# Kernel tuning notes

Measured on AMD Instinct MI355X. Metric: run time of the kernel, lower is better.

## Reference

```python
import jax, jax.numpy as jnp
import numpy as np

B, N, E = 4, 1024, 8192
NF_IN, NF_H, NF_OUT = 32, 128, 3


def _lin(key, fan_in, fan_out):
    k1, k2 = jax.random.split(key)
    bound = 1.0 / np.sqrt(fan_in)
    W = jax.random.uniform(k1, (fan_in, fan_out), jnp.float32, -bound, bound)
    b = jax.random.uniform(k2, (fan_out,), jnp.float32, -bound, bound)
    return W, b


def setup_inputs() -> dict:
    key = jax.random.key(0)
    ks = jax.random.split(key, 16)
    x = jax.random.normal(ks[0], (B, N, NF_IN), jnp.float32)
    # One-hot receiver/sender relation matrices [B, E, N]
    recv = jax.random.randint(ks[1], (B, E), 0, N)
    send = jax.random.randint(ks[2], (B, E), 0, N)
    Rr = jax.nn.one_hot(recv, N, dtype=jnp.float32)
    Rs = jax.nn.one_hot(send, N, dtype=jnp.float32)
    neW0, neb0 = _lin(ks[3], NF_IN, NF_H)
    neW1, neb1 = _lin(ks[4], NF_H, NF_H)
    neW2, neb2 = _lin(ks[5], NF_H, NF_H)
    eeW0, eeb0 = _lin(ks[6], NF_IN * 2, NF_H)
    eeW1, eeb1 = _lin(ks[7], NF_H, NF_H)
    eeW2, eeb2 = _lin(ks[8], NF_H, NF_H)
    npW, npb = _lin(ks[9], NF_H * 2, NF_H)
    epW, epb = _lin(ks[10], NF_H * 3, NF_H)
    ppW0, ppb0 = _lin(ks[11], NF_H * 2, NF_H)
    ppW1, ppb1 = _lin(ks[12], NF_H, NF_H)
    ppW2, ppb2 = _lin(ks[13], NF_H, NF_OUT)
    return dict(x=x, Rr=Rr, Rs=Rs, pstep=2,
                neW0=neW0, neb0=neb0, neW1=neW1, neb1=neb1, neW2=neW2, neb2=neb2,
                eeW0=eeW0, eeb0=eeb0, eeW1=eeW1, eeb1=eeb1, eeW2=eeW2, eeb2=eeb2,
                npW=npW, npb=npb, epW=epW, epb=epb,
                ppW0=ppW0, ppb0=ppb0, ppW1=ppW1, ppb1=ppb1, ppW2=ppW2, ppb2=ppb2)


def _encoder(x, W0, b0, W1, b1, W2, b2):
    # Linear->ReLU x3 (ReLU after last layer too)
    h = jax.nn.relu(x @ W0 + b0)
    h = jax.nn.relu(h @ W1 + b1)
    return jax.nn.relu(h @ W2 + b2)


def _predictor(x, W0, b0, W1, b1, W2, b2):
    h = jax.nn.relu(x @ W0 + b0)
    h = jax.nn.relu(h @ W1 + b1)
    return h @ W2 + b2


def reference(x, Rr, Rs, pstep,
              neW0, neb0, neW1, neb1, neW2, neb2,
              eeW0, eeb0, eeW1, eeb1, eeW2, eeb2,
              npW, npb, epW, epb,
              ppW0, ppb0, ppW1, ppb1, ppW2, ppb2):
    node_encode = _encoder(x, neW0, neb0, neW1, neb1, neW2, neb2)  # [B,N,H]
    node_effect = node_encode
    x_r = jnp.einsum('ben,bnf->bef', Rr, x)  # gather receiver features
    x_s = jnp.einsum('ben,bnf->bef', Rs, x)  # gather sender features
    edge_encode = _encoder(jnp.concatenate([x_r, x_s], -1),
                           eeW0, eeb0, eeW1, eeb1, eeW2, eeb2)  # [B,E,H]
    for _ in range(pstep):
        ne_r = jnp.einsum('ben,bnh->beh', Rr, node_effect)
        ne_s = jnp.einsum('ben,bnh->beh', Rs, node_effect)
        edge_in = jnp.concatenate([edge_encode, ne_r, ne_s], -1)  # [B,E,3H]
        edge_effect = jax.nn.relu(edge_in @ epW + epb)  # [B,E,H]
        agg = jnp.einsum('ben,beh->bnh', Rr, edge_effect)  # scatter-add to receivers
        node_in = jnp.concatenate([node_encode, agg], -1)  # [B,N,2H]
        node_effect = jax.nn.relu(node_in @ npW + npb + node_effect)  # residual
    node_reps = _predictor(jnp.concatenate([node_encode, node_effect], -1),
                           ppW0, ppb0, ppW1, ppb1, ppW2, ppb2)  # [B,N,out]
    return node_reps
```

## Files before the change

### kernel.cpp

```cpp
#include <hip/hip_runtime.h>
#include <hip/hip_bf16.h>


typedef unsigned short u16;
typedef __attribute__((ext_vector_type(8))) __bf16 bf16x8;
typedef __attribute__((ext_vector_type(4))) float f32x4;

#define N_    1024
#define BN    4096
#define BE    32768
#define LOG_E 13
#define H_    128
#define LSTR  132
#define ECAP  64
#define ASTR  136

__device__ __forceinline__ u16 f2bf(float f) {
    __bf16 h = (__bf16)f;
    return __builtin_bit_cast(u16, h);
}

__device__ __forceinline__ bf16x8 cvt8(float4 f0, float4 f1) {
    bf16x8 a;
    a[0] = (__bf16)f0.x; a[1] = (__bf16)f0.y; a[2] = (__bf16)f0.z; a[3] = (__bf16)f0.w;
    a[4] = (__bf16)f1.x; a[5] = (__bf16)f1.y; a[6] = (__bf16)f1.z; a[7] = (__bf16)f1.w;
    return a;
}

__device__ __forceinline__ bf16x8 a_from_f32(const float* p) {
    float4 f0 = *(const float4*)p;
    float4 f1 = *(const float4*)(p + 4);
    return cvt8(f0, f1);
}

__device__ __forceinline__ bf16x8 a_from_lds(const float* lds, int r, int quad, int c) {
    return a_from_f32(lds + r * LSTR + c * 32 + quad * 8);
}

__device__ __forceinline__ void mm2(const u16* __restrict__ Wf, int c, int ntb,
                                    bf16x8 a, f32x4* acc, int lane) {
    const u16* wp = Wf + ((size_t)c * 8) * 64 * 8;
    #pragma unroll
    for (int nt = 0; nt < 2; ++nt) {
        bf16x8 bw = *(const bf16x8*)(wp + (size_t)((ntb + nt) * 64 + lane) * 8);
        acc[nt] = __builtin_amdgcn_mfma_f32_16x16x32_bf16(a, bw, acc[nt], 0, 0, 0);
    }
}

__device__ __forceinline__ void zacc2(f32x4* acc) {
    acc[0] = (f32x4){0.f, 0.f, 0.f, 0.f};
    acc[1] = (f32x4){0.f, 0.f, 0.f, 0.f};
}

__device__ __forceinline__ void epi2_lds(float* lds, const f32x4* acc,
                                         const float* __restrict__ bias,
                                         int quad, int m, int ntb) {
    #pragma unroll
    for (int nt = 0; nt < 2; ++nt) {
        int col = (ntb + nt) * 16 + m;
        float bv = bias[col];
        #pragma unroll
        for (int i = 0; i < 4; ++i)
            lds[(quad * 4 + i) * LSTR + col] = fmaxf(acc[nt][i] + bv, 0.f);
    }
}

struct WDesc { const float* src; u16* dst; int K; };
struct WPack { WDesc d[10]; };

__global__ __launch_bounds__(256) void k_prep(WPack P,
                                              const float* __restrict__ Rr,
                                              const float* __restrict__ Rs,
                                              int* __restrict__ recv,
                                              int* __restrict__ send,
                                              int* __restrict__ deg,
                                              int* __restrict__ eidx) {
    int bx = blockIdx.x;
    if (bx >= 16384) {
        int t = bx - 16384;
        WDesc d = P.d[t / 192];
        int i = (t % 192) * 256 + threadIdx.x;
        if (i >= d.K * 128) return;
        int j    = i & 7;
        int lane = (i >> 3) & 63;
        int nt   = (i >> 9) & 7;
        int c    = i >> 12;
        int k = c * 32 + (lane >> 4) * 8 + j;
        int n = nt * 16 + (lane & 15);
        d.dst[i] = f2bf(d.src[k * 128 + n]);
        return;
    }
    int wave = threadIdx.x >> 6, lane = threadIdx.x & 63;
    int g = bx * 4 + wave;
    const float* src;
    int* dst;
    if (g < BE) { src = Rr + (size_t)g * N_;        dst = recv + g; }
    else        { src = Rs + (size_t)(g - BE) * N_; dst = send + (g - BE); }
    int idx = 0;
    bool done = false;
    #pragma unroll
    for (int it = 0; it < 4; ++it) {
        if (!done) {
            int base = it * 256 + lane * 4;
            float4 v = *(const float4*)(src + base);
            int found = -1;
            if      (v.x != 0.f) found = base;
            else if (v.y != 0.f) found = base + 1;
            else if (v.z != 0.f) found = base + 2;
            else if (v.w != 0.f) found = base + 3;
            unsigned long long msk = __ballot(found >= 0);
            if (msk) {
                int sl = __ffsll((long long)msk) - 1;
                idx = __shfl(found, sl, 64);
                done = true;
            }
        }
    }
    if (lane == 0) {
        *dst = idx;
        if (g < BE) {
            int node = (g >> LOG_E) * N_ + idx;
            int pos = atomicAdd(deg + node, 1);
            if (pos < ECAP) eidx[node * ECAP + pos] = g;
        }
    }
}

__global__ __launch_bounds__(256) void k_enc(
    const float* __restrict__ x,
    const int* __restrict__ recv, const int* __restrict__ send,
    const u16* __restrict__ nW0, const float* __restrict__ nb0,
    const u16* __restrict__ nW1, const float* __restrict__ nb1,
    const u16* __restrict__ nW2, const float* __restrict__ nb2,
    const u16* __restrict__ eW0, const float* __restrict__ eb0,
    const u16* __restrict__ eW1, const float* __restrict__ eb1,
    const u16* __restrict__ eW2, const float* __restrict__ eb2,
    float* __restrict__ nenc_f, u16* __restrict__ nenc_bf,
    u16* __restrict__ eenc)
{
    __shared__ float lds[2][16 * LSTR];
    int tid = threadIdx.x, lane = tid & 63, w = tid >> 6;
    int m = lane & 15, quad = lane >> 4;
    int ntb = w * 2;
    f32x4 acc[2];

    if (blockIdx.x < 256) {
        int row16 = blockIdx.x * 16;
        zacc2(acc);
        mm2(nW0, 0, ntb, a_from_f32(x + (size_t)(row16 + m) * 32 + quad * 8), acc, lane);
        epi2_lds(lds[0], acc, nb0, quad, m, ntb);
        __syncthreads();

        zacc2(acc);
        #pragma unroll
        for (int c = 0; c < 4; ++c)
            mm2(nW1, c, ntb, a_from_lds(lds[0], m, quad, c), acc, lane);
        epi2_lds(lds[1], acc, nb1, quad, m, ntb);
        __syncthreads();

        zacc2(acc);
        #pragma unroll
        for (int c = 0; c < 4; ++c)
            mm2(nW2, c, ntb, a_from_lds(lds[1], m, quad, c), acc, lane);
        epi2_lds(lds[0], acc, nb2, quad, m, ntb);
        __syncthreads();

        #pragma unroll
        for (int t = 0; t < 8; ++t) {
            int flat = t * 256 + tid, r = flat >> 7, col = flat & 127;
            nenc_f[(size_t)(row16 + r) * H_ + col] = lds[0][r * LSTR + col];
        }
        #pragma unroll
        for (int t = 0; t < 4; ++t) {
            int p = t * 256 + tid, r = p >> 6, c2 = (p & 63) * 2;
            u16 lo = f2bf(lds[0][r * LSTR + c2]);
            u16 hi = f2bf(lds[0][r * LSTR + c2 + 1]);
            *(unsigned*)(nenc_bf + (size_t)(row16 + r) * H_ + c2) =
                (unsigned)lo | ((unsigned)hi << 16);
        }
        return;
    }

    int row16 = (blockIdx.x - 256) * 16;
    int e = row16 + m, b = e >> LOG_E;
    long rr = (long)b * N_ + recv[e];
    long rs = (long)b * N_ + send[e];

    zacc2(acc);
    mm2(eW0, 0, ntb, a_from_f32(x + rr * 32 + quad * 8), acc, lane);
    mm2(eW0, 1, ntb, a_from_f32(x + rs * 32 + quad * 8), acc, lane);
    epi2_lds(lds[0], acc, eb0, quad, m, ntb);
    __syncthreads();

    zacc2(acc);
    #pragma unroll
    for (int c = 0; c < 4; ++c)
        mm2(eW1, c, ntb, a_from_lds(lds[0], m, quad, c), acc, lane);
    epi2_lds(lds[1], acc, eb1, quad, m, ntb);
    __syncthreads();

    zacc2(acc);
    #pragma unroll
    for (int c = 0; c < 4; ++c)
        mm2(eW2, c, ntb, a_from_lds(lds[1], m, quad, c), acc, lane);
    epi2_lds(lds[0], acc, eb2, quad, m, ntb);
    __syncthreads();

    #pragma unroll
    for (int t = 0; t < 4; ++t) {
        int p = t * 256 + tid, r = p >> 6, c2 = (p & 63) * 2;
        u16 lo = f2bf(lds[0][r * LSTR + c2]);
        u16 hi = f2bf(lds[0][r * LSTR + c2 + 1]);
        *(unsigned*)(eenc + (size_t)(row16 + r) * H_ + c2) =
            (unsigned)lo | ((unsigned)hi << 16);
    }
}

__global__ __launch_bounds__(256) void k_eprop(
    const u16* __restrict__ eenc, const u16* __restrict__ eff_bf,
    const int* __restrict__ recv, const int* __restrict__ send,
    const u16* __restrict__ Wf, const float* __restrict__ bias,
    float* __restrict__ edge_eff)
{
    int tid = threadIdx.x, lane = tid & 63, w = tid >> 6;
    int m = lane & 15, quad = lane >> 4;
    int row16 = blockIdx.x * 16, ntb = w * 2;
    int e = row16 + m;
    long rr = ((long)(e >> LOG_E) * N_ + recv[e]) * H_;
    long rs = ((long)(e >> LOG_E) * N_ + send[e]) * H_;
    f32x4 acc[2];
    zacc2(acc);

    #pragma unroll
    for (int c = 0; c < 4; ++c)
        mm2(Wf, c, ntb,
            *(const bf16x8*)(eenc + (size_t)e * H_ + c * 32 + quad * 8), acc, lane);
    #pragma unroll
    for (int c = 0; c < 4; ++c)
        mm2(Wf, 4 + c, ntb,
            *(const bf16x8*)(eff_bf + rr + c * 32 + quad * 8), acc, lane);
    #pragma unroll
    for (int c = 0; c < 4; ++c)
        mm2(Wf, 8 + c, ntb,
            *(const bf16x8*)(eff_bf + rs + c * 32 + quad * 8), acc, lane);

    #pragma unroll
    for (int nt = 0; nt < 2; ++nt) {
        int col = (ntb + nt) * 16 + m;
        float bv = bias[col];
        #pragma unroll
        for (int i = 0; i < 4; ++i)
            edge_eff[(size_t)(row16 + quad * 4 + i) * H_ + col] =
                fmaxf(acc[nt][i] + bv, 0.f);
    }
}

__device__ __forceinline__ void gather_agg(u16* aggl, int row16, int tid, int lane,
                                           const float* __restrict__ edge_eff,
                                           const int* __restrict__ deg,
                                           const int* __restrict__ eidx) {
    int nd = tid >> 4, l = tid & 15;
    int node = row16 + nd;
    int dg = deg[node]; dg = dg < ECAP ? dg : ECAP;
    int ev = eidx[node * ECAP + l];
    int base = lane & 48;
    float s[8] = {0.f, 0.f, 0.f, 0.f, 0.f, 0.f, 0.f, 0.f};
    int d16 = dg < 16 ? dg : 16;
    int t = 0;
    for (; t + 1 < d16; t += 2) {
        int e0 = __shfl(ev, base | t, 64);
        int e1 = __shfl(ev, base | (t + 1), 64);
        const float* p0 = edge_eff + (size_t)e0 * H_ + l * 8;
        const float* p1 = edge_eff + (size_t)e1 * H_ + l * 8;
        float4 a0 = *(const float4*)p0, b0 = *(const float4*)(p0 + 4);
        float4 a1 = *(const float4*)p1, b1 = *(const float4*)(p1 + 4);
        s[0] += a0.x + a1.x; s[1] += a0.y + a1.y;
        s[2] += a0.z + a1.z; s[3] += a0.w + a1.w;
        s[4] += b0.x + b1.x; s[5] += b0.y + b1.y;
        s[6] += b0.z + b1.z; s[7] += b0.w + b1.w;
    }
    if (t < d16) {
        int e0 = __shfl(ev, base | t, 64);
        const float* p0 = edge_eff + (size_t)e0 * H_ + l * 8;
        float4 a0 = *(const float4*)p0, b0 = *(const float4*)(p0 + 4);
        s[0] += a0.x; s[1] += a0.y; s[2] += a0.z; s[3] += a0.w;
        s[4] += b0.x; s[5] += b0.y; s[6] += b0.z; s[7] += b0.w;
        ++t;
    }
    for (; t < dg; ++t) {
        int e0 = eidx[node * ECAP + t];
        const float* p0 = edge_eff + (size_t)e0 * H_ + l * 8;
        float4 a0 = *(const float4*)p0, b0 = *(const float4*)(p0 + 4);
        s[0] += a0.x; s[1] += a0.y; s[2] += a0.z; s[3] += a0.w;
        s[4] += b0.x; s[5] += b0.y; s[6] += b0.z; s[7] += b0.w;
    }
    bf16x8 o;
    #pragma unroll
    for (int j = 0; j < 8; ++j) o[j] = (__bf16)s[j];
    *(bf16x8*)(aggl + nd * ASTR + l * 8) = o;
}

__global__ __launch_bounds__(256) void k_nprop(
    const u16* __restrict__ nenc_bf, const float* __restrict__ edge_eff,
    const int* __restrict__ deg, const int* __restrict__ eidx,
    const float* __restrict__ eff_f,
    const u16* __restrict__ Wf, const float* __restrict__ bias,
    float* __restrict__ nout_f, u16* __restrict__ nout_bf)
{
    __shared__ u16 aggl[16 * ASTR];
    int tid = threadIdx.x, lane = tid & 63, w = tid >> 6;
    int m = lane & 15, quad = lane >> 4;
    int row16 = blockIdx.x * 16;

    gather_agg(aggl, row16, tid, lane, edge_eff, deg, eidx);
    __syncthreads();

    int row = row16 + m, ntb = w * 2;
    f32x4 acc[2];
    zacc2(acc);
    #pragma unroll
    for (int c = 0; c < 4; ++c)
        mm2(Wf, c, ntb,
            *(const bf16x8*)(nenc_bf + (size_t)row * H_ + c * 32 + quad * 8), acc, lane);
    #pragma unroll
    for (int c = 0; c < 4; ++c)
        mm2(Wf, 4 + c, ntb,
            *(const bf16x8*)(aggl + m * ASTR + c * 32 + quad * 8), acc, lane);

    #pragma unroll
    for (int nt = 0; nt < 2; ++nt) {
        int col = (ntb + nt) * 16 + m;
        float bv = bias[col];
        #pragma unroll
        for (int i = 0; i < 4; ++i) {
            int r = row16 + quad * 4 + i;
            float v = fmaxf(acc[nt][i] + bv + eff_f[(size_t)r * H_ + col], 0.f);
            nout_f[(size_t)r * H_ + col] = v;
            nout_bf[(size_t)r * H_ + col] = f2bf(v);
        }
    }
}

__global__ __launch_bounds__(256) void k_npropred(
    const u16* __restrict__ nenc_bf, const float* __restrict__ edge_eff,
    const int* __restrict__ deg, const int* __restrict__ eidx,
    const float* __restrict__ eff_f,
    const u16* __restrict__ Wnp, const float* __restrict__ bnp,
    const u16* __restrict__ Wp0, const float* __restrict__ bp0,
    const u16* __restrict__ Wp1, const float* __restrict__ bp1,
    const float* __restrict__ W2, const float* __restrict__ b2,
    float* __restrict__ out)
{
    __shared__ u16 aggl[16 * ASTR];
    __shared__ u16 vl[16 * ASTR];
    __shared__ u16 h1[16 * ASTR];
    __shared__ float h2[16 * LSTR];
    int tid = threadIdx.x, lane = tid & 63, w = tid >> 6;
    int m = lane & 15, quad = lane >> 4;
    int row16 = blockIdx.x * 16;

    gather_agg(aggl, row16, tid, lane, edge_eff, deg, eidx);
    __syncthreads();

    int row = row16 + m, ntb = w * 2;
    f32x4 acc[2];

    zacc2(acc);
    #pragma unroll
    for (int c = 0; c < 4; ++c)
        mm2(Wnp, c, ntb,
            *(const bf16x8*)(nenc_bf + (size_t)row * H_ + c * 32 + quad * 8), acc, lane);
    #pragma unroll
    for (int c = 0; c < 4; ++c)
        mm2(Wnp, 4 + c, ntb,
            *(const bf16x8*)(aggl + m * ASTR + c * 32 + quad * 8), acc, lane);
    #pragma unroll
    for (int nt = 0; nt < 2; ++nt) {
        int col = (ntb + nt) * 16 + m;
        float bv = bnp[col];
        #pragma unroll
        for (int i = 0; i < 4; ++i) {
            int r = quad * 4 + i;
            float v = fmaxf(acc[nt][i] + bv + eff_f[(size_t)(row16 + r) * H_ + col], 0.f);
            vl[r * ASTR + col] = f2bf(v);
        }
    }
    __syncthreads();

    zacc2(acc);
    #pragma unroll
    for (int c = 0; c < 4; ++c)
        mm2(Wp0, c, ntb,
            *(const bf16x8*)(nenc_bf + (size_t)row * H_ + c * 32 + quad * 8), acc, lane);
    #pragma unroll
    for (int c = 0; c < 4; ++c)
        mm2(Wp0, 4 + c, ntb,
            *(const bf16x8*)(vl + m * ASTR + c * 32 + quad * 8), acc, lane);
    #pragma unroll
    for (int nt = 0; nt < 2; ++nt) {
        int col = (ntb + nt) * 16 + m;
        float bv = bp0[col];
        #pragma unroll
        for (int i = 0; i < 4; ++i)
            h1[(quad * 4 + i) * ASTR + col] = f2bf(fmaxf(acc[nt][i] + bv, 0.f));
    }
    __syncthreads();

    zacc2(acc);
    #pragma unroll
    for (int c = 0; c < 4; ++c)
        mm2(Wp1, c, ntb,
            *(const bf16x8*)(h1 + m * ASTR + c * 32 + quad * 8), acc, lane);
    #pragma unroll
    for (int nt = 0; nt < 2; ++nt) {
        int col = (ntb + nt) * 16 + m;
        float bv = bp1[col];
        #pragma unroll
        for (int i = 0; i < 4; ++i)
            h2[(quad * 4 + i) * LSTR + col] = fmaxf(acc[nt][i] + bv, 0.f);
    }
    __syncthreads();

    if (w == 0) {
        int r = lane & 15, col = lane >> 4;
        if (col < 3) {
            float s = 0.f;
            #pragma unroll 8
            for (int k = 0; k < 128; ++k)
                s += h2[r * LSTR + k] * W2[k * 3 + col];
            out[(size_t)(row16 + r) * 3 + col] = s + b2[col];
        }
    }
}

extern "C" void kernel_launch(void* const* d_in, const int* in_sizes, int n_in,
                              void* d_out, int out_size, void* d_ws, size_t ws_size,
                              hipStream_t stream) {
    (void)in_sizes; (void)n_in; (void)out_size; (void)ws_size;

    const float* x    = (const float*)d_in[0];
    const float* Rr   = (const float*)d_in[1];
    const float* Rs   = (const float*)d_in[2];
    const float* neW0 = (const float*)d_in[4];  const float* neb0 = (const float*)d_in[5];
    const float* neW1 = (const float*)d_in[6];  const float* neb1 = (const float*)d_in[7];
    const float* neW2 = (const float*)d_in[8];  const float* neb2 = (const float*)d_in[9];
    const float* eeW0 = (const float*)d_in[10]; const float* eeb0 = (const float*)d_in[11];
    const float* eeW1 = (const float*)d_in[12]; const float* eeb1 = (const float*)d_in[13];
    const float* eeW2 = (const float*)d_in[14]; const float* eeb2 = (const float*)d_in[15];
    const float* npW  = (const float*)d_in[16]; const float* npb  = (const float*)d_in[17];
    const float* epW  = (const float*)d_in[18]; const float* epb  = (const float*)d_in[19];
    const float* ppW0 = (const float*)d_in[20]; const float* ppb0 = (const float*)d_in[21];
    const float* ppW1 = (const float*)d_in[22]; const float* ppb1 = (const float*)d_in[23];
    const float* ppW2 = (const float*)d_in[24]; const float* ppb2 = (const float*)d_in[25];

    char* ws = (char*)d_ws;
    size_t off = 0;
    auto alloc = [&](size_t bytes) -> char* {
        char* p = ws + off;
        off += (bytes + 255) & ~(size_t)255;
        return p;
    };

    u16* f_neW0 = (u16*)alloc(32  * 128 * 2);
    u16* f_neW1 = (u16*)alloc(128 * 128 * 2);
    u16* f_neW2 = (u16*)alloc(128 * 128 * 2);
    u16* f_eeW0 = (u16*)alloc(64  * 128 * 2);
    u16* f_eeW1 = (u16*)alloc(128 * 128 * 2);
    u16* f_eeW2 = (u16*)alloc(128 * 128 * 2);
    u16* f_epW  = (u16*)alloc(384 * 128 * 2);
    u16* f_npW  = (u16*)alloc(256 * 128 * 2);
    u16* f_ppW0 = (u16*)alloc(256 * 128 * 2);
    u16* f_ppW1 = (u16*)alloc(128 * 128 * 2);
    int*   recv = (int*)alloc(BE * 4);
    int*   send = (int*)alloc(BE * 4);
    int*   deg  = (int*)alloc(BN * 4);
    int*   eidx = (int*)alloc((size_t)BN * ECAP * 4);
    float* nenc_f  = (float*)alloc((size_t)BN * H_ * 4);
    u16*   nenc_bf = (u16*)alloc((size_t)BN * H_ * 2);
    float* nef1_f  = (float*)alloc((size_t)BN * H_ * 4);
    u16*   nef1_bf = (u16*)alloc((size_t)BN * H_ * 2);
    float* edge_eff = (float*)alloc((size_t)BE * H_ * 4);
    u16*   eenc = (u16*)alloc((size_t)BE * H_ * 2);

    WPack P;
    P.d[0] = {neW0, f_neW0, 32};
    P.d[1] = {neW1, f_neW1, 128};
    P.d[2] = {neW2, f_neW2, 128};
    P.d[3] = {eeW0, f_eeW0, 64};
    P.d[4] = {eeW1, f_eeW1, 128};
    P.d[5] = {eeW2, f_eeW2, 128};
    P.d[6] = {epW,  f_epW,  384};
    P.d[7] = {npW,  f_npW,  256};
    P.d[8] = {ppW0, f_ppW0, 256};
    P.d[9] = {ppW1, f_ppW1, 128};

    hipMemsetAsync(deg, 0, BN * 4, stream);

    k_prep<<<16384 + 1920, 256, 0, stream>>>(P, Rr, Rs, recv, send, deg, eidx);

    k_enc<<<256 + 2048, 256, 0, stream>>>(x, recv, send,
                                          f_neW0, neb0, f_neW1, neb1, f_neW2, neb2,
                                          f_eeW0, eeb0, f_eeW1, eeb1, f_eeW2, eeb2,
                                          nenc_f, nenc_bf, eenc);

    k_eprop<<<BE / 16, 256, 0, stream>>>(eenc, nenc_bf, recv, send, f_epW, epb, edge_eff);
    k_nprop<<<BN / 16, 256, 0, stream>>>(nenc_bf, edge_eff, deg, eidx, nenc_f,
                                         f_npW, npb, nef1_f, nef1_bf);
    k_eprop<<<BE / 16, 256, 0, stream>>>(eenc, nef1_bf, recv, send, f_epW, epb, edge_eff);
    k_npropred<<<BN / 16, 256, 0, stream>>>(nenc_bf, edge_eff, deg, eidx, nef1_f,
                                            f_npW, npb, f_ppW0, ppb0, f_ppW1, ppb1,
                                            ppW2, ppb2, (float*)d_out);
}
```

Baseline: 383.4 us.

## Stage weights in LDS and give each wave 16 edge rows across all 128 columns

The edge encoder and edge propagation kernels change their work split. Before, each block handled 16 edges and each wave computed 2 of the 8 column tiles, reading its weight fragments straight from global memory. Now each block handles 64 edges, each wave owns 16 rows across all 8 column tiles, and each weight matrix is staged cooperatively into LDS in chunks. The aim is to cut redundant global weight traffic and to reuse each gathered A fragment for 8 MFMAs. The cost is more accumulator registers, extra barriers between staging steps, and a quarter as many blocks. Node blocks are reordered to come after the edge blocks in the encoder launch.

```diff
diff --git a/kernel.cpp b/kernel.cpp
--- a/kernel.cpp
+++ b/kernel.cpp
@@ -37,6 +37,16 @@
     return a_from_f32(lds + r * LSTR + c * 32 + quad * 8);
 }
 
+__device__ __forceinline__ void mm8L(const u16* wb, int cc, bf16x8 a,
+                                     f32x4* acc, int lane) {
+    const u16* wp = wb + cc * 4096;
+    #pragma unroll
+    for (int nt = 0; nt < 8; ++nt) {
+        bf16x8 bw = *(const bf16x8*)(wp + (nt * 64 + lane) * 8);
+        acc[nt] = __builtin_amdgcn_mfma_f32_16x16x32_bf16(a, bw, acc[nt], 0, 0, 0);
+    }
+}
+
 __device__ __forceinline__ void mm2(const u16* __restrict__ Wf, int c, int ntb,
                                     bf16x8 a, f32x4* acc, int lane) {
     const u16* wp = Wf + ((size_t)c * 8) * 64 * 8;
@@ -47,9 +57,32 @@
     }
 }
 
+__device__ __forceinline__ void zacc8(f32x4* acc) {
+    #pragma unroll
+    for (int t = 0; t < 8; ++t) acc[t] = (f32x4){0.f, 0.f, 0.f, 0.f};
+}
 __device__ __forceinline__ void zacc2(f32x4* acc) {
     acc[0] = (f32x4){0.f, 0.f, 0.f, 0.f};
     acc[1] = (f32x4){0.f, 0.f, 0.f, 0.f};
+}
+
+__device__ __forceinline__ void stage_w(u16* dst, const u16* __restrict__ src,
+                                        int n16, int tid) {
+    for (int t = tid; t < n16; t += 256)
+        *(bf16x8*)(dst + t * 8) = *(const bf16x8*)(src + t * 8);
+}
+
+__device__ __forceinline__ void epi8_bf(u16* t, const f32x4* acc,
+                                        const float* __restrict__ bias,
+                                        int quad, int m) {
+    #pragma unroll
+    for (int nt = 0; nt < 8; ++nt) {
+        float bv = bias[nt * 16 + m];
+        #pragma unroll
+        for (int i = 0; i < 4; ++i)
+            t[(quad * 4 + i) * ASTR + nt * 16 + m] =
+                f2bf(fmaxf(acc[nt][i] + bv, 0.f));
+    }
 }
 
 __device__ __forceinline__ void epi2_lds(float* lds, const f32x4* acc,
@@ -138,80 +171,100 @@
     float* __restrict__ nenc_f, u16* __restrict__ nenc_bf,
     u16* __restrict__ eenc)
 {
-    __shared__ float lds[2][16 * LSTR];
+    __shared__ union U {
+        struct { u16 wbuf[8192]; u16 tile[4][2][16 * ASTR]; } e;
+        struct { float lds[2][16 * LSTR]; } n;
+    } sm;
     int tid = threadIdx.x, lane = tid & 63, w = tid >> 6;
     int m = lane & 15, quad = lane >> 4;
-    int ntb = w * 2;
+
+    if (blockIdx.x < 512) {
+        int myrow16 = blockIdx.x * 64 + w * 16;
+        int e = myrow16 + m, b = e >> LOG_E;
+        long rr = (long)b * N_ + recv[e];
+        long rs = (long)b * N_ + send[e];
+        u16* t0 = sm.e.tile[w][0];
+        u16* t1 = sm.e.tile[w][1];
+        f32x4 acc[8];
+
+        stage_w(sm.e.wbuf, eW0, 1024, tid);
+        __syncthreads();
+        zacc8(acc);
+        mm8L(sm.e.wbuf, 0, a_from_f32(x + rr * 32 + quad * 8), acc, lane);
+        mm8L(sm.e.wbuf, 1, a_from_f32(x + rs * 32 + quad * 8), acc, lane);
+        epi8_bf(t0, acc, eb0, quad, m);
+        __syncthreads();
+
+        zacc8(acc);
+        #pragma unroll
+        for (int h = 0; h < 2; ++h) {
+            stage_w(sm.e.wbuf, eW1 + h * 8192, 1024, tid);
+            __syncthreads();
+            #pragma unroll
+            for (int cp = 0; cp < 2; ++cp) {
+                int c = h * 2 + cp;
+                bf16x8 a = *(const bf16x8*)(t0 + m * ASTR + c * 32 + quad * 8);
+                mm8L(sm.e.wbuf, cp, a, acc, lane);
+            }
+            __syncthreads();
+        }
+        epi8_bf(t1, acc, eb1, quad, m);
+
+        zacc8(acc);
+        #pragma unroll
+        for (int h = 0; h < 2; ++h) {
+            stage_w(sm.e.wbuf, eW2 + h * 8192, 1024, tid);
+            __syncthreads();
+            #pragma unroll
+            for (int cp = 0; cp < 2; ++cp) {
+                int c = h * 2 + cp;
+                bf16x8 a = *(const bf16x8*)(t1 + m * ASTR + c * 32 + quad * 8);
+                mm8L(sm.e.wbuf, cp, a, acc, lane);
+            }
+            __syncthreads();
+        }
+        epi8_bf(t0, acc, eb2, quad, m);
+
+        #pragma unroll
+        for (int t = 0; t < 16; ++t)
+            *(unsigned*)(eenc + (size_t)(myrow16 + t) * H_ + lane * 2) =
+                *(const unsigned*)(t0 + t * ASTR + lane * 2);
+        return;
+    }
+
+    int row16 = (blockIdx.x - 512) * 16, ntb = w * 2;
     f32x4 acc[2];
 
-    if (blockIdx.x < 256) {
-        int row16 = blockIdx.x * 16;
-        zacc2(acc);
-        mm2(nW0, 0, ntb, a_from_f32(x + (size_t)(row16 + m) * 32 + quad * 8), acc, lane);
-        epi2_lds(lds[0], acc, nb0, quad, m, ntb);
-        __syncthreads();
-
-        zacc2(acc);
-        #pragma unroll
-        for (int c = 0; c < 4; ++c)
-            mm2(nW1, c, ntb, a_from_lds(lds[0], m, quad, c), acc, lane);
-        epi2_lds(lds[1], acc, nb1, quad, m, ntb);
-        __syncthreads();
-
-        zacc2(acc);
-        #pragma unroll
-        for (int c = 0; c < 4; ++c)
-            mm2(nW2, c, ntb, a_from_lds(lds[1], m, quad, c), acc, lane);
-        epi2_lds(lds[0], acc, nb2, quad, m, ntb);
-        __syncthreads();
-
-        #pragma unroll
-        for (int t = 0; t < 8; ++t) {
-            int flat = t * 256 + tid, r = flat >> 7, col = flat & 127;
-            nenc_f[(size_t)(row16 + r) * H_ + col] = lds[0][r * LSTR + col];
-        }
-        #pragma unroll
-        for (int t = 0; t < 4; ++t) {
-            int p = t * 256 + tid, r = p >> 6, c2 = (p & 63) * 2;
-            u16 lo = f2bf(lds[0][r * LSTR + c2]);
-            u16 hi = f2bf(lds[0][r * LSTR + c2 + 1]);
-            *(unsigned*)(nenc_bf + (size_t)(row16 + r) * H_ + c2) =
-                (unsigned)lo | ((unsigned)hi << 16);
-        }
-        return;
-    }
-
-    int row16 = (blockIdx.x - 256) * 16;
-    int e = row16 + m, b = e >> LOG_E;
-    long rr = (long)b * N_ + recv[e];
-    long rs = (long)b * N_ + send[e];
-
-    zacc2(acc);
-    mm2(eW0, 0, ntb, a_from_f32(x + rr * 32 + quad * 8), acc, lane);
-    mm2(eW0, 1, ntb, a_from_f32(x + rs * 32 + quad * 8), acc, lane);
-    epi2_lds(lds[0], acc, eb0, quad, m, ntb);
-    __syncthreads();
-
-    zacc2(acc);
-    #pragma unroll
-    for (int c = 0; c < 4; ++c)
-        mm2(eW1, c, ntb, a_from_lds(lds[0], m, quad, c), acc, lane);
-    epi2_lds(lds[1], acc, eb1, quad, m, ntb);
-    __syncthreads();
-
-    zacc2(acc);
-    #pragma unroll
-    for (int c = 0; c < 4; ++c)
-        mm2(eW2, c, ntb, a_from_lds(lds[1], m, quad, c), acc, lane);
-    epi2_lds(lds[0], acc, eb2, quad, m, ntb);
-    __syncthreads();
-
+    zacc2(acc);
+    mm2(nW0, 0, ntb, a_from_f32(x + (size_t)(row16 + m) * 32 + quad * 8), acc, lane);
+    epi2_lds(sm.n.lds[0], acc, nb0, quad, m, ntb);
+    __syncthreads();
+
+    zacc2(acc);
+    #pragma unroll
+    for (int c = 0; c < 4; ++c)
+        mm2(nW1, c, ntb, a_from_lds(sm.n.lds[0], m, quad, c), acc, lane);
+    epi2_lds(sm.n.lds[1], acc, nb1, quad, m, ntb);
+    __syncthreads();
+
+    zacc2(acc);
+    #pragma unroll
+    for (int c = 0; c < 4; ++c)
+        mm2(nW2, c, ntb, a_from_lds(sm.n.lds[1], m, quad, c), acc, lane);
+    epi2_lds(sm.n.lds[0], acc, nb2, quad, m, ntb);
+    __syncthreads();
+
+    #pragma unroll
+    for (int t = 0; t < 8; ++t) {
+        int flat = t * 256 + tid, r = flat >> 7, col = flat & 127;
+        nenc_f[(size_t)(row16 + r) * H_ + col] = sm.n.lds[0][r * LSTR + col];
+    }
     #pragma unroll
     for (int t = 0; t < 4; ++t) {
         int p = t * 256 + tid, r = p >> 6, c2 = (p & 63) * 2;
-        u16 lo = f2bf(lds[0][r * LSTR + c2]);
-        u16 hi = f2bf(lds[0][r * LSTR + c2 + 1]);
-        *(unsigned*)(eenc + (size_t)(row16 + r) * H_ + c2) =
+        u16 lo = f2bf(sm.n.lds[0][r * LSTR + c2]);
+        u16 hi = f2bf(sm.n.lds[0][r * LSTR + c2 + 1]);
+        *(unsigned*)(nenc_bf + (size_t)(row16 + r) * H_ + c2) =
             (unsigned)lo | ((unsigned)hi << 16);
     }
 }
@@ -222,35 +275,38 @@
     const u16* __restrict__ Wf, const float* __restrict__ bias,
     float* __restrict__ edge_eff)
 {
+    __shared__ u16 wbuf[16384];
     int tid = threadIdx.x, lane = tid & 63, w = tid >> 6;
     int m = lane & 15, quad = lane >> 4;
-    int row16 = blockIdx.x * 16, ntb = w * 2;
-    int e = row16 + m;
+    int myrow16 = blockIdx.x * 64 + w * 16;
+    int e = myrow16 + m;
     long rr = ((long)(e >> LOG_E) * N_ + recv[e]) * H_;
     long rs = ((long)(e >> LOG_E) * N_ + send[e]) * H_;
-    f32x4 acc[2];
-    zacc2(acc);
-
-    #pragma unroll
-    for (int c = 0; c < 4; ++c)
-        mm2(Wf, c, ntb,
-            *(const bf16x8*)(eenc + (size_t)e * H_ + c * 32 + quad * 8), acc, lane);
-    #pragma unroll
-    for (int c = 0; c < 4; ++c)
-        mm2(Wf, 4 + c, ntb,
-            *(const bf16x8*)(eff_bf + rr + c * 32 + quad * 8), acc, lane);
-    #pragma unroll
-    for (int c = 0; c < 4; ++c)
-        mm2(Wf, 8 + c, ntb,
-            *(const bf16x8*)(eff_bf + rs + c * 32 + quad * 8), acc, lane);
-
-    #pragma unroll
-    for (int nt = 0; nt < 2; ++nt) {
-        int col = (ntb + nt) * 16 + m;
+    f32x4 acc[8];
+    zacc8(acc);
+
+    #pragma unroll
+    for (int g = 0; g < 3; ++g) {
+        stage_w(wbuf, Wf + g * 16384, 2048, tid);
+        __syncthreads();
+        const u16* abase = (g == 0) ? eenc + (size_t)e * H_
+                         : (g == 1) ? eff_bf + rr
+                                    : eff_bf + rs;
+        #pragma unroll
+        for (int c = 0; c < 4; ++c) {
+            bf16x8 a = *(const bf16x8*)(abase + c * 32 + quad * 8);
+            mm8L(wbuf, c, a, acc, lane);
+        }
+        __syncthreads();
+    }
+
+    #pragma unroll
+    for (int nt = 0; nt < 8; ++nt) {
+        int col = nt * 16 + m;
         float bv = bias[col];
         #pragma unroll
         for (int i = 0; i < 4; ++i)
-            edge_eff[(size_t)(row16 + quad * 4 + i) * H_ + col] =
+            edge_eff[(size_t)(myrow16 + quad * 4 + i) * H_ + col] =
                 fmaxf(acc[nt][i] + bv, 0.f);
     }
 }
@@ -498,15 +554,15 @@
 
     k_prep<<<16384 + 1920, 256, 0, stream>>>(P, Rr, Rs, recv, send, deg, eidx);
 
-    k_enc<<<256 + 2048, 256, 0, stream>>>(x, recv, send,
-                                          f_neW0, neb0, f_neW1, neb1, f_neW2, neb2,
-                                          f_eeW0, eeb0, f_eeW1, eeb1, f_eeW2, eeb2,
-                                          nenc_f, nenc_bf, eenc);
-
-    k_eprop<<<BE / 16, 256, 0, stream>>>(eenc, nenc_bf, recv, send, f_epW, epb, edge_eff);
+    k_enc<<<512 + 256, 256, 0, stream>>>(x, recv, send,
+                                         f_neW0, neb0, f_neW1, neb1, f_neW2, neb2,
+                                         f_eeW0, eeb0, f_eeW1, eeb1, f_eeW2, eeb2,
+                                         nenc_f, nenc_bf, eenc);
+
+    k_eprop<<<BE / 64, 256, 0, stream>>>(eenc, nenc_bf, recv, send, f_epW, epb, edge_eff);
     k_nprop<<<BN / 16, 256, 0, stream>>>(nenc_bf, edge_eff, deg, eidx, nenc_f,
                                          f_npW, npb, nef1_f, nef1_bf);
-    k_eprop<<<BE / 16, 256, 0, stream>>>(eenc, nef1_bf, recv, send, f_epW, epb, edge_eff);
+    k_eprop<<<BE / 64, 256, 0, stream>>>(eenc, nef1_bf, recv, send, f_epW, epb, edge_eff);
     k_npropred<<<BN / 16, 256, 0, stream>>>(nenc_bf, edge_eff, deg, eidx, nef1_f,
                                             f_npW, npb, f_ppW0, ppb0, f_ppW1, ppb1,
                                             ppW2, ppb2, (float*)d_out);
```

Result: faster. 365.4 us (median of 2 runs) (-4.7%).
